# Optimization experiments

Measured on AMD Instinct MI355X. Metric: run time of the kernel, lower is better.

## Reference

```python
import jax, jax.numpy as jnp
import numpy as np

N_NODES = 50000
N_EDGES = 800000
N_GRAPHS = 64
IN_C, HID_C, OUT_C = 768, 128, 1


def setup_inputs() -> dict:
    key = jax.random.key(0)
    ks = jax.random.split(key, 9)
    x = jax.random.normal(ks[0], (N_NODES, IN_C), dtype=jnp.float32)
    edge_index = jax.random.randint(ks[1], (2, N_EDGES), 0, N_NODES, dtype=jnp.int32)
    batch = jnp.sort(jax.random.randint(ks[2], (N_NODES,), 0, N_GRAPHS, dtype=jnp.int32))
    s1 = 1.0 / np.sqrt(IN_C)
    s2 = 1.0 / np.sqrt(HID_C)
    W1 = jax.random.normal(ks[3], (IN_C, HID_C), dtype=jnp.float32) * s1
    b1 = jnp.zeros((HID_C,), dtype=jnp.float32)
    W2 = jax.random.normal(ks[4], (HID_C, HID_C), dtype=jnp.float32) * s2
    b2 = jnp.zeros((HID_C,), dtype=jnp.float32)
    Wl = jax.random.normal(ks[5], (HID_C, OUT_C), dtype=jnp.float32) * s2
    bl = jnp.zeros((OUT_C,), dtype=jnp.float32)
    return {"x": x, "edge_index": edge_index, "batch": batch,
            "W1": W1, "b1": b1, "W2": W2, "b2": b2, "Wl": Wl, "bl": bl}


def gcn_conv(x, W, b, src, dst, n_nodes):
    """PyG GCNConv: linear transform, symmetric norm with self-loops, scatter-add."""
    xl = x @ W  # [N, C_out]
    # in-degree including self-loop
    deg = jax.ops.segment_sum(jnp.ones_like(dst, dtype=xl.dtype), dst,
                              num_segments=n_nodes) + 1.0
    dinv = jax.lax.rsqrt(deg)  # deg >= 1 so safe
    norm = dinv[src] * dinv[dst]  # [E]
    agg = jax.ops.segment_sum(norm[:, None] * xl[src], dst, num_segments=n_nodes)
    # self-loop message: dinv[i]^2 * xl[i]
    agg = agg + xl * (dinv * dinv)[:, None]
    return agg + b


def reference(x, edge_index, batch, W1, b1, W2, b2, Wl, bl):
    src, dst = edge_index[0], edge_index[1]
    n = x.shape[0]
    h = jax.nn.relu(gcn_conv(x, W1, b1, src, dst, n))
    # dropout is identity in eval mode
    h = jax.nn.relu(gcn_conv(h, W2, b2, src, dst, n))
    # global mean pool over graphs
    sums = jax.ops.segment_sum(h, batch, num_segments=N_GRAPHS)
    cnts = jax.ops.segment_sum(jnp.ones((n,), dtype=h.dtype), batch,
                               num_segments=N_GRAPHS)
    pooled = sums / jnp.maximum(cnts, 1.0)[:, None]
    return pooled @ Wl + bl
```

## Files before the change

kernel.cpp:

```cpp
#include <hip/hip_runtime.h>

#define N_NODES  50000
#define N_EDGES  800000
#define N_GRAPHS 64
#define N_CHUNK  4
#define ZREP     16
#define SCAN_BLOCKS 196
#define GATHER_BLOCKS 1568

typedef unsigned short u16x8 __attribute__((ext_vector_type(8)));
typedef short s16x8 __attribute__((ext_vector_type(8)));
typedef float f32x4 __attribute__((ext_vector_type(4)));

__device__ __forceinline__ float bf2f(unsigned short h) {
    return __uint_as_float((unsigned)h << 16);
}
__device__ __forceinline__ unsigned short f2bf(float f) {
    unsigned u = __float_as_uint(f);
    unsigned r = (u + 0x7FFFu + ((u >> 16) & 1u)) >> 16;
    return (unsigned short)r;
}
__device__ __forceinline__ unsigned pk2(float a, float b) {
    return (unsigned)f2bf(a) | ((unsigned)f2bf(b) << 16);
}


__global__ void zero_int_kernel(int* __restrict__ p, int n) {
    for (int i = blockIdx.x * blockDim.x + threadIdx.x; i < n; i += gridDim.x * blockDim.x)
        p[i] = 0;
}

__global__ void hist_kernel(const int* __restrict__ ei, int* __restrict__ cnt) {
    const int* dst = ei + N_EDGES;
    for (int e = blockIdx.x * blockDim.x + threadIdx.x; e < N_EDGES; e += gridDim.x * blockDim.x)
        atomicAdd(&cnt[dst[e]], 1);
}

__global__ void scanA_kernel(const int* __restrict__ cnt, int* __restrict__ bsum,
                             float* __restrict__ dinv) {
    __shared__ int wsum[4];
    int t = threadIdx.x;
    int i = blockIdx.x * 256 + t;
    int v = cnt[i];
    if (i < N_NODES) dinv[i] = rsqrtf((float)v + 1.f);
    int s = v;
    #pragma unroll
    for (int off = 1; off < 64; off <<= 1) s += __shfl_xor(s, off);
    if ((t & 63) == 0) wsum[t >> 6] = s;
    __syncthreads();
    if (t == 0) bsum[blockIdx.x] = wsum[0] + wsum[1] + wsum[2] + wsum[3];
}

__global__ void scanB_kernel(const int* __restrict__ bsum, int* __restrict__ boff,
                             const int* __restrict__ batch, float* __restrict__ cntg,
                             float* __restrict__ zsumR) {
    __shared__ int wsum[4];
    int t = threadIdx.x;
    int lane = t & 63, w = t >> 6;
    int v = (t < SCAN_BLOCKS) ? bsum[t] : 0;
    int s = v;
    #pragma unroll
    for (int off = 1; off < 64; off <<= 1) {
        int u = __shfl_up(s, off);
        if (lane >= off) s += u;
    }
    if (lane == 63) wsum[w] = s;
    __syncthreads();
    int wo = 0;
    for (int j = 0; j < w; ++j) wo += wsum[j];
    if (t < SCAN_BLOCKS) boff[t] = wo + s - v;

    if (t < N_GRAPHS) {
        #pragma unroll
        for (int r = 0; r < ZREP; ++r) zsumR[r * N_GRAPHS + t] = 0.f;
        int g = t;
        int lo = 0, hi = N_NODES;
        while (lo < hi) { int mid = (lo + hi) >> 1; if (batch[mid] < g) lo = mid + 1; else hi = mid; }
        int a = lo;
        lo = 0; hi = N_NODES;
        while (lo < hi) { int mid = (lo + hi) >> 1; if (batch[mid] < g + 1) lo = mid + 1; else hi = mid; }
        cntg[g] = (float)(lo - a);
    }
}

__global__ void scanC_kernel(int* __restrict__ cnt, const int* __restrict__ boff,
                             int* __restrict__ rowptr) {
    __shared__ int wsum[4];
    int t = threadIdx.x;
    int i = blockIdx.x * 256 + t;
    int lane = t & 63, w = t >> 6;
    int v = cnt[i];
    int s = v;
    #pragma unroll
    for (int off = 1; off < 64; off <<= 1) {
        int u = __shfl_up(s, off);
        if (lane >= off) s += u;
    }
    if (lane == 63) wsum[w] = s;
    __syncthreads();
    int wo = 0;
    for (int j = 0; j < w; ++j) wo += wsum[j];
    rowptr[i] = boff[blockIdx.x] + wo + s - v;
    cnt[i] = 0;
}

__global__ void fill_kernel(const int* __restrict__ ei, const int* __restrict__ rowptr,
                            int* __restrict__ fill, const float* __restrict__ dinv,
                            int2* __restrict__ csr) {
    const int* src = ei;
    const int* dst = ei + N_EDGES;
    for (int e = blockIdx.x * blockDim.x + threadIdx.x; e < N_EDGES; e += gridDim.x * blockDim.x) {
        int s = src[e], d = dst[e];
        int pos = rowptr[d] + atomicAdd(&fill[d], 1);
        csr[pos] = make_int2(s, __float_as_int(dinv[s] * dinv[d]));
    }
}

__global__ void prep_w_kernel(const float* __restrict__ W1, const float* __restrict__ W2,
                              unsigned short* __restrict__ w1h, unsigned short* __restrict__ w1l,
                              unsigned short* __restrict__ w2h, unsigned short* __restrict__ w2l) {
    const int n1 = 768 * 128, n2 = 128 * 128;
    for (int i = blockIdx.x * blockDim.x + threadIdx.x; i < n1 + n2; i += gridDim.x * blockDim.x) {
        if (i < n1) {
            int k = i >> 7, c = i & 127;
            float w = W1[i];
            unsigned short hi = f2bf(w);
            unsigned short lo = f2bf(w - bf2f(hi));
            w1h[c * 768 + k] = hi;
            w1l[c * 768 + k] = lo;
        } else {
            int j = i - n1;
            int k = j >> 7, c = j & 127;
            float w = W2[j];
            unsigned short hi = f2bf(w);
            unsigned short lo = f2bf(w - bf2f(hi));
            w2h[c * 128 + k] = hi;
            w2l[c * 128 + k] = lo;
        }
    }
}

template<int K, bool BF16A>
__global__ __launch_bounds__(256) void gemm_mfma(const void* __restrict__ Av,
                                                 const unsigned short* __restrict__ Wth,
                                                 const unsigned short* __restrict__ Wtl,
                                                 unsigned short* __restrict__ C, int M) {
    __shared__ unsigned short Xs[128 * 40];
    __shared__ unsigned short Wh[128 * 40];
    __shared__ unsigned short Wl[128 * 40];

    const int tid  = threadIdx.x;
    const int row0 = blockIdx.x * 128;
    const int trow  = tid >> 1;
    const int thalf = (tid & 1) * 16;

    int grow = row0 + trow;
    if (grow >= M) grow = M - 1;
    const float* xpf = (const float*)Av + (long)grow * K + thalf;
    const unsigned short* xpb = (const unsigned short*)Av + (long)grow * K + thalf;
    const unsigned short* wph = Wth + (long)trow * K + thalf;
    const unsigned short* wpl = Wtl + (long)trow * K + thalf;

    f32x4 acc[8][2];
    #pragma unroll
    for (int rf = 0; rf < 8; ++rf)
        #pragma unroll
        for (int cf = 0; cf < 2; ++cf)
            acc[rf][cf] = (f32x4){0.f, 0.f, 0.f, 0.f};

    float4 f0, f1, f2, f3;
    uint4 xb0, xb1;
    if constexpr (!BF16A) {
        f0 = *(const float4*)(xpf);
        f1 = *(const float4*)(xpf + 4);
        f2 = *(const float4*)(xpf + 8);
        f3 = *(const float4*)(xpf + 12);
    } else {
        xb0 = *(const uint4*)(xpb);
        xb1 = *(const uint4*)(xpb + 8);
    }
    uint4 wh0 = ((const uint4*)(wph))[0];
    uint4 wh1 = ((const uint4*)(wph))[1];
    uint4 wl0 = ((const uint4*)(wpl))[0];
    uint4 wl1 = ((const uint4*)(wpl))[1];

    const int l   = tid & 63;
    const int wv  = tid >> 6;
    const int lr  = l & 15;
    const int lk8 = (l >> 4) * 8;

    for (int k0 = 0; k0 < K; k0 += 32) {
        unsigned short* xrow = &Xs[trow * 40 + thalf];
        if constexpr (!BF16A) {
            *(uint4*)(xrow)     = make_uint4(pk2(f0.x, f0.y), pk2(f0.z, f0.w), pk2(f1.x, f1.y), pk2(f1.z, f1.w));
            *(uint4*)(xrow + 8) = make_uint4(pk2(f2.x, f2.y), pk2(f2.z, f2.w), pk2(f3.x, f3.y), pk2(f3.z, f3.w));
        } else {
            *(uint4*)(xrow)     = xb0;
            *(uint4*)(xrow + 8) = xb1;
        }
        *(uint4*)&Wh[trow * 40 + thalf]     = wh0;
        *(uint4*)&Wh[trow * 40 + thalf + 8] = wh1;
        *(uint4*)&Wl[trow * 40 + thalf]     = wl0;
        *(uint4*)&Wl[trow * 40 + thalf + 8] = wl1;
        __syncthreads();

        if (k0 + 32 < K) {
            if constexpr (!BF16A) {
                f0 = *(const float4*)(xpf + k0 + 32);
                f1 = *(const float4*)(xpf + k0 + 36);
                f2 = *(const float4*)(xpf + k0 + 40);
                f3 = *(const float4*)(xpf + k0 + 44);
            } else {
                xb0 = *(const uint4*)(xpb + k0 + 32);
                xb1 = *(const uint4*)(xpb + k0 + 40);
            }
            wh0 = ((const uint4*)(wph + k0 + 32))[0];
            wh1 = ((const uint4*)(wph + k0 + 32))[1];
            wl0 = ((const uint4*)(wpl + k0 + 32))[0];
            wl1 = ((const uint4*)(wpl + k0 + 32))[1];
        }

        s16x8 xb[8], whf[2], wlf[2];
        #pragma unroll
        for (int rf = 0; rf < 8; ++rf)
            xb[rf] = *(const s16x8*)&Xs[(rf * 16 + lr) * 40 + lk8];
        #pragma unroll
        for (int cf = 0; cf < 2; ++cf) {
            whf[cf] = *(const s16x8*)&Wh[(wv * 32 + cf * 16 + lr) * 40 + lk8];
            wlf[cf] = *(const s16x8*)&Wl[(wv * 32 + cf * 16 + lr) * 40 + lk8];
        }
        #pragma unroll
        for (int rf = 0; rf < 8; ++rf)
            #pragma unroll
            for (int cf = 0; cf < 2; ++cf) {
                acc[rf][cf] = __builtin_amdgcn_mfma_f32_16x16x32_bf16(wlf[cf], xb[rf], acc[rf][cf], 0, 0, 0);
                acc[rf][cf] = __builtin_amdgcn_mfma_f32_16x16x32_bf16(whf[cf], xb[rf], acc[rf][cf], 0, 0, 0);
            }
        __syncthreads();
    }

    const int c4 = (l >> 4) * 4;
    #pragma unroll
    for (int rf = 0; rf < 8; ++rf) {
        int r = row0 + rf * 16 + lr;
        if (r < M) {
            #pragma unroll
            for (int cf = 0; cf < 2; ++cf) {
                int cb = wv * 32 + cf * 16 + c4;
                ushort4 v;
                v.x = f2bf(acc[rf][cf][0]);
                v.y = f2bf(acc[rf][cf][1]);
                v.z = f2bf(acc[rf][cf][2]);
                v.w = f2bf(acc[rf][cf][3]);
                *(ushort4*)(C + ((long)(cb >> 5) * N_NODES + r) * 32 + (cb & 31)) = v;
            }
        }
    }
}

template<int MODE>
__global__ __launch_bounds__(256, 6) void gather_all_kernel(
        const unsigned short* __restrict__ xlc, const float* __restrict__ dinv,
        const int* __restrict__ rowptr, const int2* __restrict__ csr,
        const float* __restrict__ bias, unsigned short* __restrict__ outbuf,
        const float* __restrict__ Wl, const int* __restrict__ batch,
        float* __restrict__ zsumR) {
    const int lane = threadIdx.x & 63;
    const int half = lane & 1;
    const int c0   = half * 16;

    const int grp   = blockIdx.x & 7;
    const int chunk = grp & 3;
    const unsigned short* xc = xlc + (long)chunk * N_NODES * 32;

    const int cblk = (blockIdx.x >> 3) + (grp >> 2) * 196;
    const int wvc  = cblk * 4 + (threadIdx.x >> 6);
    const int slot = wvc * 32 + (lane >> 1);
    const bool vn  = slot < N_NODES;
    const int node = vn ? slot : N_NODES - 1;

    const int start = rowptr[node];
    const int end   = vn ? rowptr[node + 1] : start;
    const float di  = dinv[node];

    const u16x8* srow = (const u16x8*)(xc + (long)node * 32 + c0);
    u16x8 s0 = srow[0], s1 = srow[1];

    float acc[16];
    #pragma unroll
    for (int j = 0; j < 16; ++j) acc[j] = 0.f;

    int e = start;
    for (; e + 3 < end; e += 4) {
        int2 cA = csr[e];
        int2 cB = csr[e + 1];
        int2 cC = csr[e + 2];
        int2 cD = csr[e + 3];
        float wA = __int_as_float(cA.y);
        float wB = __int_as_float(cB.y);
        float wC = __int_as_float(cC.y);
        float wD = __int_as_float(cD.y);
        const u16x8* rA = (const u16x8*)(xc + (long)cA.x * 32 + c0);
        const u16x8* rB = (const u16x8*)(xc + (long)cB.x * 32 + c0);
        const u16x8* rC = (const u16x8*)(xc + (long)cC.x * 32 + c0);
        const u16x8* rD = (const u16x8*)(xc + (long)cD.x * 32 + c0);
        u16x8 a0 = rA[0], a1 = rA[1];
        u16x8 b0 = rB[0], b1 = rB[1];
        u16x8 d0 = rC[0], d1 = rC[1];
        u16x8 e0 = rD[0], e1 = rD[1];
        #pragma unroll
        for (int j = 0; j < 8; ++j) {
            acc[j]     = fmaf(wA, bf2f(a0[j]), acc[j]);
            acc[j + 8] = fmaf(wA, bf2f(a1[j]), acc[j + 8]);
        }
        #pragma unroll
        for (int j = 0; j < 8; ++j) {
            acc[j]     = fmaf(wB, bf2f(b0[j]), acc[j]);
            acc[j + 8] = fmaf(wB, bf2f(b1[j]), acc[j + 8]);
        }
        #pragma unroll
        for (int j = 0; j < 8; ++j) {
            acc[j]     = fmaf(wC, bf2f(d0[j]), acc[j]);
            acc[j + 8] = fmaf(wC, bf2f(d1[j]), acc[j + 8]);
        }
        #pragma unroll
        for (int j = 0; j < 8; ++j) {
            acc[j]     = fmaf(wD, bf2f(e0[j]), acc[j]);
            acc[j + 8] = fmaf(wD, bf2f(e1[j]), acc[j + 8]);
        }
    }
    for (; e < end; ++e) {
        int2 cA = csr[e];
        float wA = __int_as_float(cA.y);
        const u16x8* rA = (const u16x8*)(xc + (long)cA.x * 32 + c0);
        u16x8 a0 = rA[0], a1 = rA[1];
        #pragma unroll
        for (int j = 0; j < 8; ++j) {
            acc[j]     = fmaf(wA, bf2f(a0[j]), acc[j]);
            acc[j + 8] = fmaf(wA, bf2f(a1[j]), acc[j + 8]);
        }
    }

    const float w2 = di * di;
    const float* bch = bias + chunk * 32 + c0;
    float s[16];
    #pragma unroll
    for (int j = 0; j < 8; ++j) {
        s[j]     = fmaxf(fmaf(w2, bf2f(s0[j]), acc[j])     + bch[j],     0.f);
        s[j + 8] = fmaxf(fmaf(w2, bf2f(s1[j]), acc[j + 8]) + bch[j + 8], 0.f);
    }

    if (MODE == 0) {
        if (vn) {
            unsigned short* op = outbuf + (long)node * 128 + chunk * 32 + c0;
            u16x8 o0, o1;
            #pragma unroll
            for (int j = 0; j < 8; ++j) {
                o0[j] = f2bf(s[j]);
                o1[j] = f2bf(s[j + 8]);
            }
            ((u16x8*)op)[0] = o0;
            ((u16x8*)op)[1] = o1;
        }
    } else {
        const float* wch = Wl + chunk * 32 + c0;
        float z = 0.f;
        #pragma unroll
        for (int j = 0; j < 16; ++j) z = fmaf(s[j], wch[j], z);
        z += __shfl_xor(z, 1);
        if (!vn || half) z = 0.f;
        int b = batch[node];
        int b0v = __shfl(b, 0);
        bool uniform = __all(b == b0v);
        if (uniform) {
            #pragma unroll
            for (int off = 1; off < 64; off <<= 1) z += __shfl_xor(z, off);
            if (lane == 0)
                atomicAdd(&zsumR[(blockIdx.x & (ZREP - 1)) * N_GRAPHS + b0v], z);
        } else if (vn && !half) {
            atomicAdd(&zsumR[((lane >> 1) & (ZREP - 1)) * N_GRAPHS + b], z);
        }
    }
}

__global__ void out_kernel(const float* __restrict__ zsumR, const float* __restrict__ cntg,
                           const float* __restrict__ bl, float* __restrict__ out) {
    int g = threadIdx.x;
    if (g < N_GRAPHS) {
        float z = 0.f;
        #pragma unroll
        for (int r = 0; r < ZREP; ++r) z += zsumR[r * N_GRAPHS + g];
        out[g] = z / fmaxf(cntg[g], 1.f) + bl[0];
    }
}


extern "C" void kernel_launch(void* const* d_in, const int* in_sizes, int n_in,
                              void* d_out, int out_size, void* d_ws, size_t ws_size,
                              hipStream_t stream) {
    const float* x    = (const float*)d_in[0];
    const int*   ei   = (const int*)d_in[1];
    const int*   batch= (const int*)d_in[2];
    const float* W1   = (const float*)d_in[3];
    const float* b1   = (const float*)d_in[4];
    const float* W2   = (const float*)d_in[5];
    const float* b2   = (const float*)d_in[6];
    const float* Wl   = (const float*)d_in[7];
    const float* bl   = (const float*)d_in[8];
    float* out = (float*)d_out;

    float* ws      = (float*)d_ws;
    float* dinv    = ws;
    float* zsumR   = ws + 50176;
    float* cntg    = ws + 51200;
    int*   cnt_i   = (int*)(ws + 51264);
    int*   rowptr  = (int*)(ws + 101440);
    int2*  csr     = (int2*)(ws + 151616);
    unsigned short* xl16 = (unsigned short*)(ws + 1751616);
    unsigned short* h1   = (unsigned short*)(ws + 1751616 + 3200000);
    unsigned short* w1h = (unsigned short*)(ws + 11351616);
    unsigned short* w1l = w1h + 98304;
    unsigned short* w2h = w1l + 98304;
    unsigned short* w2l = w2h + 16384;
    int* bsum = (int*)(w2l + 16384);
    int* boff = bsum + 256;

    zero_int_kernel<<<128, 256, 0, stream>>>(cnt_i, 50176);

    hist_kernel<<<1024, 256, 0, stream>>>(ei, cnt_i);
    scanA_kernel<<<SCAN_BLOCKS, 256, 0, stream>>>(cnt_i, bsum, dinv);
    scanB_kernel<<<1, 256, 0, stream>>>(bsum, boff, batch, cntg, zsumR);
    scanC_kernel<<<SCAN_BLOCKS, 256, 0, stream>>>(cnt_i, boff, rowptr);
    fill_kernel<<<1024, 256, 0, stream>>>(ei, rowptr, cnt_i, dinv, csr);
    prep_w_kernel<<<448, 256, 0, stream>>>(W1, W2, w1h, w1l, w2h, w2l);

    gemm_mfma<768, false><<<391, 256, 0, stream>>>(x, w1h, w1l, xl16, N_NODES);
    gather_all_kernel<0><<<GATHER_BLOCKS, 256, 0, stream>>>(
        xl16, dinv, rowptr, csr, b1, h1, nullptr, nullptr, nullptr);

    gemm_mfma<128, true><<<391, 256, 0, stream>>>(h1, w2h, w2l, xl16, N_NODES);
    gather_all_kernel<1><<<GATHER_BLOCKS, 256, 0, stream>>>(
        xl16, dinv, rowptr, csr, b2, nullptr, Wl, batch, zsumR);

    out_kernel<<<1, 64, 0, stream>>>(zsumR, cntg, bl, out);
}
```

Baseline: 236.5 us.

## Split GEMM tiles across two column blocks, enlarge gather grid, use memset

Each GEMM block now computes a 128x64 output tile instead of 128x128, and the grid doubles to 782 blocks. This is meant to give more blocks per CU and better load balance, at the cost of reading each A row tile twice, relying on the L2 cache to absorb the repeat. The gather grid grows from 1568 to 2048 blocks with matching slot mapping, which adds blocks that have no nodes to process. The custom zeroing kernel is replaced with hipMemsetAsync.

```diff
diff --git a/kernel.cpp b/kernel.cpp
--- a/kernel.cpp
+++ b/kernel.cpp
@@ -6,7 +6,7 @@
 #define N_CHUNK  4
 #define ZREP     16
 #define SCAN_BLOCKS 196
-#define GATHER_BLOCKS 1568
+#define GATHER_BLOCKS 2048
 
 typedef unsigned short u16x8 __attribute__((ext_vector_type(8)));
 typedef short s16x8 __attribute__((ext_vector_type(8)));
@@ -24,11 +24,6 @@
     return (unsigned)f2bf(a) | ((unsigned)f2bf(b) << 16);
 }
 
-
-__global__ void zero_int_kernel(int* __restrict__ p, int n) {
-    for (int i = blockIdx.x * blockDim.x + threadIdx.x; i < n; i += gridDim.x * blockDim.x)
-        p[i] = 0;
-}
 
 __global__ void hist_kernel(const int* __restrict__ ei, int* __restrict__ cnt) {
     const int* dst = ei + N_EDGES;
@@ -146,27 +141,31 @@
                                                  const unsigned short* __restrict__ Wtl,
                                                  unsigned short* __restrict__ C, int M) {
     __shared__ unsigned short Xs[128 * 40];
-    __shared__ unsigned short Wh[128 * 40];
-    __shared__ unsigned short Wl[128 * 40];
+    __shared__ unsigned short Wh[64 * 40];
+    __shared__ unsigned short Wl[64 * 40];
 
     const int tid  = threadIdx.x;
-    const int row0 = blockIdx.x * 128;
+    const int rowblk = blockIdx.x >> 1;
+    const int colblk = blockIdx.x & 1;
+    const int row0 = rowblk * 128;
+    const int col0 = colblk * 64;
+
     const int trow  = tid >> 1;
     const int thalf = (tid & 1) * 16;
-
     int grow = row0 + trow;
     if (grow >= M) grow = M - 1;
     const float* xpf = (const float*)Av + (long)grow * K + thalf;
     const unsigned short* xpb = (const unsigned short*)Av + (long)grow * K + thalf;
-    const unsigned short* wph = Wth + (long)trow * K + thalf;
-    const unsigned short* wpl = Wtl + (long)trow * K + thalf;
-
-    f32x4 acc[8][2];
+
+    const int wc  = tid >> 2;
+    const int wk8 = (tid & 3) * 8;
+    const unsigned short* wph = Wth + (long)(col0 + wc) * K + wk8;
+    const unsigned short* wpl = Wtl + (long)(col0 + wc) * K + wk8;
+
+    f32x4 acc[8];
     #pragma unroll
     for (int rf = 0; rf < 8; ++rf)
-        #pragma unroll
-        for (int cf = 0; cf < 2; ++cf)
-            acc[rf][cf] = (f32x4){0.f, 0.f, 0.f, 0.f};
+        acc[rf] = (f32x4){0.f, 0.f, 0.f, 0.f};
 
     float4 f0, f1, f2, f3;
     uint4 xb0, xb1;
@@ -179,10 +178,8 @@
         xb0 = *(const uint4*)(xpb);
         xb1 = *(const uint4*)(xpb + 8);
     }
-    uint4 wh0 = ((const uint4*)(wph))[0];
-    uint4 wh1 = ((const uint4*)(wph))[1];
-    uint4 wl0 = ((const uint4*)(wpl))[0];
-    uint4 wl1 = ((const uint4*)(wpl))[1];
+    uint4 whr = *(const uint4*)(wph);
+    uint4 wlr = *(const uint4*)(wpl);
 
     const int l   = tid & 63;
     const int wv  = tid >> 6;
@@ -198,10 +195,8 @@
             *(uint4*)(xrow)     = xb0;
             *(uint4*)(xrow + 8) = xb1;
         }
-        *(uint4*)&Wh[trow * 40 + thalf]     = wh0;
-        *(uint4*)&Wh[trow * 40 + thalf + 8] = wh1;
-        *(uint4*)&Wl[trow * 40 + thalf]     = wl0;
-        *(uint4*)&Wl[trow * 40 + thalf + 8] = wl1;
+        *(uint4*)&Wh[wc * 40 + wk8] = whr;
+        *(uint4*)&Wl[wc * 40 + wk8] = wlr;
         __syncthreads();
 
         if (k0 + 32 < K) {
@@ -214,28 +209,21 @@
                 xb0 = *(const uint4*)(xpb + k0 + 32);
                 xb1 = *(const uint4*)(xpb + k0 + 40);
             }
-            wh0 = ((const uint4*)(wph + k0 + 32))[0];
-            wh1 = ((const uint4*)(wph + k0 + 32))[1];
-            wl0 = ((const uint4*)(wpl + k0 + 32))[0];
-            wl1 = ((const uint4*)(wpl + k0 + 32))[1];
-        }
-
-        s16x8 xb[8], whf[2], wlf[2];
+            whr = *(const uint4*)(wph + k0 + 32);
+            wlr = *(const uint4*)(wpl + k0 + 32);
+        }
+
+        s16x8 xb[8], whf, wlf;
         #pragma unroll
         for (int rf = 0; rf < 8; ++rf)
             xb[rf] = *(const s16x8*)&Xs[(rf * 16 + lr) * 40 + lk8];
-        #pragma unroll
-        for (int cf = 0; cf < 2; ++cf) {
-            whf[cf] = *(const s16x8*)&Wh[(wv * 32 + cf * 16 + lr) * 40 + lk8];
-            wlf[cf] = *(const s16x8*)&Wl[(wv * 32 + cf * 16 + lr) * 40 + lk8];
-        }
-        #pragma unroll
-        for (int rf = 0; rf < 8; ++rf)
-            #pragma unroll
-            for (int cf = 0; cf < 2; ++cf) {
-                acc[rf][cf] = __builtin_amdgcn_mfma_f32_16x16x32_bf16(wlf[cf], xb[rf], acc[rf][cf], 0, 0, 0);
-                acc[rf][cf] = __builtin_amdgcn_mfma_f32_16x16x32_bf16(whf[cf], xb[rf], acc[rf][cf], 0, 0, 0);
-            }
+        whf = *(const s16x8*)&Wh[(wv * 16 + lr) * 40 + lk8];
+        wlf = *(const s16x8*)&Wl[(wv * 16 + lr) * 40 + lk8];
+        #pragma unroll
+        for (int rf = 0; rf < 8; ++rf) {
+            acc[rf] = __builtin_amdgcn_mfma_f32_16x16x32_bf16(wlf, xb[rf], acc[rf], 0, 0, 0);
+            acc[rf] = __builtin_amdgcn_mfma_f32_16x16x32_bf16(whf, xb[rf], acc[rf], 0, 0, 0);
+        }
         __syncthreads();
     }
 
@@ -244,16 +232,13 @@
     for (int rf = 0; rf < 8; ++rf) {
         int r = row0 + rf * 16 + lr;
         if (r < M) {
-            #pragma unroll
-            for (int cf = 0; cf < 2; ++cf) {
-                int cb = wv * 32 + cf * 16 + c4;
-                ushort4 v;
-                v.x = f2bf(acc[rf][cf][0]);
-                v.y = f2bf(acc[rf][cf][1]);
-                v.z = f2bf(acc[rf][cf][2]);
-                v.w = f2bf(acc[rf][cf][3]);
-                *(ushort4*)(C + ((long)(cb >> 5) * N_NODES + r) * 32 + (cb & 31)) = v;
-            }
+            int cb = col0 + wv * 16 + c4;
+            ushort4 v;
+            v.x = f2bf(acc[rf][0]);
+            v.y = f2bf(acc[rf][1]);
+            v.z = f2bf(acc[rf][2]);
+            v.w = f2bf(acc[rf][3]);
+            *(ushort4*)(C + ((long)(cb >> 5) * N_NODES + r) * 32 + (cb & 31)) = v;
         }
     }
 }
@@ -273,7 +258,7 @@
     const int chunk = grp & 3;
     const unsigned short* xc = xlc + (long)chunk * N_NODES * 32;
 
-    const int cblk = (blockIdx.x >> 3) + (grp >> 2) * 196;
+    const int cblk = (blockIdx.x >> 3) + (grp >> 2) * 256;
     const int wvc  = cblk * 4 + (threadIdx.x >> 6);
     const int slot = wvc * 32 + (lane >> 1);
     const bool vn  = slot < N_NODES;
@@ -425,7 +410,7 @@
     int* bsum = (int*)(w2l + 16384);
     int* boff = bsum + 256;
 
-    zero_int_kernel<<<128, 256, 0, stream>>>(cnt_i, 50176);
+    hipMemsetAsync(cnt_i, 0, 50176 * sizeof(int), stream);
 
     hist_kernel<<<1024, 256, 0, stream>>>(ei, cnt_i);
     scanA_kernel<<<SCAN_BLOCKS, 256, 0, stream>>>(cnt_i, bsum, dinv);
@@ -434,11 +419,11 @@
     fill_kernel<<<1024, 256, 0, stream>>>(ei, rowptr, cnt_i, dinv, csr);
     prep_w_kernel<<<448, 256, 0, stream>>>(W1, W2, w1h, w1l, w2h, w2l);
 
-    gemm_mfma<768, false><<<391, 256, 0, stream>>>(x, w1h, w1l, xl16, N_NODES);
+    gemm_mfma<768, false><<<782, 256, 0, stream>>>(x, w1h, w1l, xl16, N_NODES);
     gather_all_kernel<0><<<GATHER_BLOCKS, 256, 0, stream>>>(
         xl16, dinv, rowptr, csr, b1, h1, nullptr, nullptr, nullptr);
 
-    gemm_mfma<128, true><<<391, 256, 0, stream>>>(h1, w2h, w2l, xl16, N_NODES);
+    gemm_mfma<128, true><<<782, 256, 0, stream>>>(h1, w2h, w2l, xl16, N_NODES);
     gather_all_kernel<1><<<GATHER_BLOCKS, 256, 0, stream>>>(
         xl16, dinv, rowptr, csr, b2, nullptr, Wl, batch, zsumR);
 
```

New measurement: 267.7 us. 13.2% more time.
